# Kernel tuning notes

Hardware: AMD Instinct MI355X
Metric: run time of the kernel (lower is better)

The kernel has to match this reference:

```python
import jax, jax.numpy as jnp
import numpy as np

POOL_RATIOS = [0.5, 0.5, 0.5]
N_NODES = 100000
N_EDGES = 3200000
D = 1443  # hard-coded feature dim in the module


def setup_inputs() -> dict:
    key = jax.random.key(0)
    ks = jax.random.split(key, 6)
    x = jax.random.normal(ks[0], (N_NODES, D), dtype=jnp.float32)
    edge_index = jax.random.randint(ks[1], (2, N_EDGES), 0, N_NODES, dtype=jnp.int64)
    edge_attr = jax.random.uniform(ks[2], (N_EDGES,), dtype=jnp.float32)
    w1 = jax.random.normal(ks[3], (D,), dtype=jnp.float32)
    w2 = jax.random.normal(ks[4], (D,), dtype=jnp.float32)
    w3 = jax.random.normal(ks[5], (D,), dtype=jnp.float32)
    return {"x": x, "edge_index": edge_index, "edge_attr": edge_attr,
            "w1": w1, "w2": w2, "w3": w3}


def _topk_pool(x, w, ratio, n):
    # PyG TopKPooling (single graph, batch = zeros):
    #   score = tanh((x @ attn) / ||attn||); perm = top-k(score, ceil(ratio*N));
    #   x_out = x[perm] * score[perm][:, None]
    s = jnp.tanh((x @ w) / jnp.linalg.norm(w))  # [n]
    k = int(np.ceil(ratio * n))                 # static per layer
    top_s, perm = jax.lax.top_k(s, k)
    return x[perm] * top_s[:, None], k


def reference(x, edge_index, edge_attr, w1, w2, w3):
    # edge_index / edge_attr never influence pooled output (edge filtering is
    # dead code w.r.t. data.x in the original module); scores depend only on x.
    n = x.shape[0]
    for w, r in zip((w1, w2, w3), POOL_RATIOS):
        x, n = _topk_pool(x, w, r, n)
    # global_mean_pool with batch == zeros -> single-graph mean, shape [1, D]
    return jnp.mean(x, axis=0, keepdims=True)
```

## Files before the change

kernel.cpp:

```cpp
#include <hip/hip_runtime.h>
#include <math.h>

#define D_FEAT 1443
#define N0     100000
#define K1SEL  50000
#define K2SEL  25000
#define K3SEL  12500
#define NB     65536
#define EQCAP  4096


__device__ __forceinline__ unsigned fkey(float f) {
    unsigned u = __float_as_uint(f);
    return (u & 0x80000000u) ? ~u : (u | 0x80000000u);
}

__global__ __launch_bounds__(256) void init_kernel(
    const float* __restrict__ w1, const float* __restrict__ w2,
    const float* __restrict__ w3,
    unsigned* __restrict__ hist1, unsigned* __restrict__ hist2,
    int* __restrict__ st, float* __restrict__ out, int outN)
{
    int gid = blockIdx.x * 256 + threadIdx.x;
    int gsz = gridDim.x * 256;
    for (int i = gid; i < NB; i += gsz) { hist1[i] = 0u; hist2[i] = 0u; }
    for (int i = gid; i < outN; i += gsz) out[i] = 0.0f;
    if (blockIdx.x == 0) {
        __shared__ double red[4];
        const float* ws_[3] = { w1, w2, w3 };
        for (int r = 0; r < 3; r++) {
            double nl = 0.0;
            for (int j = threadIdx.x; j < D_FEAT; j += 256) {
                double wv = (double)ws_[r][j]; nl += wv * wv;
            }
            for (int off = 32; off > 0; off >>= 1) nl += __shfl_down(nl, off);
            if ((threadIdx.x & 63) == 0) red[threadIdx.x >> 6] = nl;
            __syncthreads();
            if (threadIdx.x == 0)
                ((float*)st)[8 + r] = (float)(1.0 / sqrt(red[0] + red[1] + red[2] + red[3]));
            __syncthreads();
        }
        if (threadIdx.x < 8) st[threadIdx.x] = 0;
    }
}

__global__ __launch_bounds__(256) void dots_kernel(
    const float* __restrict__ x,
    const float* __restrict__ w1, const float* __restrict__ w2,
    const float* __restrict__ w3,
    float* __restrict__ d2, float* __restrict__ d3,
    unsigned* __restrict__ keys, float* __restrict__ sv,
    unsigned* __restrict__ hist1, const int* __restrict__ st)
{
    int wave = threadIdx.x >> 6, lane = threadIdx.x & 63;
    int row = blockIdx.x * 4 + wave;
    if (row >= N0) return;
    const float* xr = x + (long)row * D_FEAT;
    double a1 = 0.0, a2 = 0.0, a3 = 0.0;
    for (int j = lane; j < D_FEAT; j += 64) {
        double xv = (double)xr[j];
        a1 += xv * (double)w1[j];
        a2 += xv * (double)w2[j];
        a3 += xv * (double)w3[j];
    }
    for (int off = 32; off > 0; off >>= 1) {
        a1 += __shfl_down(a1, off);
        a2 += __shfl_down(a2, off);
        a3 += __shfl_down(a3, off);
    }
    if (lane == 0) {
        d2[row] = (float)a2;
        d3[row] = (float)a3;
        float invN = ((const float*)st)[8];
        float s = tanhf((float)a1 * invN);
        sv[row] = s;
        unsigned key = fkey(s);
        keys[row] = key;
        atomicAdd(&hist1[key >> 16], 1u);
    }
}

__global__ __launch_bounds__(256) void score_kernel(
    const float* __restrict__ dvec, const int* __restrict__ idxIn,
    const float* __restrict__ cumIn, int n, int wIdx,
    unsigned* __restrict__ keys, float* __restrict__ sv,
    unsigned* __restrict__ hist1, const int* __restrict__ st)
{
    int gid = blockIdx.x * 256 + threadIdx.x;
    if (gid >= n) return;
    float invN = ((const float*)st)[8 + wIdx];
    int row = idxIn[gid];
    float c = cumIn[gid];
    float s = tanhf(c * dvec[row] * invN);
    sv[gid] = s;
    unsigned key = fkey(s);
    keys[gid] = key;
    atomicAdd(&hist1[key >> 16], 1u);
}

__global__ __launch_bounds__(256) void hist2_kernel(
    const unsigned* __restrict__ keys, int n,
    unsigned* __restrict__ hist2, const int* __restrict__ st)
{
    int gid = blockIdx.x * 256 + threadIdx.x;
    if (gid >= n) return;
    unsigned p1 = (unsigned)st[0];
    unsigned k = keys[gid];
    if ((k >> 16) == p1) atomicAdd(&hist2[k & 0xFFFFu], 1u);
}

__global__ __launch_bounds__(1024) void pick_kernel(
    const unsigned* __restrict__ hist, int* __restrict__ st, int level, int k0)
{
    __shared__ unsigned csuf[1024];
    int tid = threadIdx.x;
    unsigned kRem = (level == 1) ? (unsigned)k0 : (unsigned)st[2];
    int base = tid * 64;
    unsigned s = 0;
    for (int b = 0; b < 64; b++) s += hist[base + b];
    csuf[tid] = s;
    __syncthreads();
    for (int off = 1; off < 1024; off <<= 1) {
        unsigned v = csuf[tid] + ((tid + off < 1024) ? csuf[tid + off] : 0u);
        __syncthreads();
        csuf[tid] = v;
        __syncthreads();
    }
    unsigned suf = csuf[tid];
    unsigned sufNext = (tid < 1023) ? csuf[tid + 1] : 0u;
    if (suf >= kRem && sufNext < kRem) {
        unsigned acc = sufNext, hsel = 0; int sel = base;
        for (int b = base + 63; b >= base; b--) {
            unsigned h = hist[b];
            acc += h;
            if (acc >= kRem) { sel = b; hsel = h; break; }
        }
        unsigned needNext = kRem - (acc - hsel);
        if (level == 1) {
            st[0] = sel;
            st[2] = (int)needNext;
        } else {
            st[1] = (int)(((unsigned)st[0] << 16) | (unsigned)sel);
            st[2] = (int)needNext;
            st[3] = (int)hsel;
            st[4] = 0;
            st[5] = 0;
        }
    }
}

__global__ __launch_bounds__(256) void compact_kernel(
    const unsigned* __restrict__ keys, const float* __restrict__ sv,
    const int* __restrict__ idxIn, const float* __restrict__ cumIn,
    int n, int* __restrict__ idxOut, float* __restrict__ cumOut,
    int* __restrict__ st,
    unsigned* __restrict__ hist1, unsigned* __restrict__ hist2, int doZero)
{
    int gid = blockIdx.x * 256 + threadIdx.x;
    int gsz = gridDim.x * 256;
    if (doZero) {
        for (int i = gid; i < NB; i += gsz) { hist1[i] = 0u; hist2[i] = 0u; }
    }
    if (gid >= n) return;
    unsigned thr = (unsigned)st[1];
    unsigned key = keys[gid];
    if (key > thr) {
        int pos = atomicAdd(&st[5], 1);
        idxOut[pos] = idxIn ? idxIn[gid] : gid;
        cumOut[pos] = (idxIn ? cumIn[gid] : 1.0f) * sv[gid];
    } else if (key == thr) {
        int e = atomicAdd(&st[4], 1);
        if (e < EQCAP) st[16 + e] = gid;
    }
}

__global__ __launch_bounds__(256) void tie_kernel(
    const float* __restrict__ sv, const int* __restrict__ idxIn,
    const float* __restrict__ cumIn, int k,
    int* __restrict__ idxOut, float* __restrict__ cumOut, int* __restrict__ st)
{
    int cnt = st[4]; if (cnt > EQCAP) cnt = EQCAP;
    int need = st[2];
    int base = k - need;
    for (int e = threadIdx.x; e < cnt; e += 256) {
        int pos = st[16 + e];
        int rank = 0;
        for (int e2 = 0; e2 < cnt; e2++) rank += (st[16 + e2] < pos) ? 1 : 0;
        if (rank < need) {
            idxOut[base + rank] = idxIn ? idxIn[pos] : pos;
            cumOut[base + rank] = (idxIn ? cumIn[pos] : 1.0f) * sv[pos];
        }
    }
}

#define WS_ROWS 64
__global__ __launch_bounds__(256) void wsum_kernel(
    const float* __restrict__ x, const int* __restrict__ idx3,
    const float* __restrict__ cum3, float* __restrict__ out)
{
    int col = blockIdx.x * 256 + threadIdx.x;
    int r0 = blockIdx.y * WS_ROWS;
    int r1 = r0 + WS_ROWS; if (r1 > K3SEL) r1 = K3SEL;
    float acc = 0.0f;
    for (int r = r0; r < r1; r++) {
        int row = idx3[r];
        float wgt = cum3[r];
        if (col < D_FEAT) acc += wgt * x[(long)row * D_FEAT + col];
    }
    if (col < D_FEAT) atomicAdd(&out[col], acc * (1.0f / (float)K3SEL));
}

extern "C" void kernel_launch(void* const* d_in, const int* in_sizes, int n_in,
                              void* d_out, int out_size, void* d_ws, size_t ws_size,
                              hipStream_t stream) {
    const float* x  = (const float*)d_in[0];
    const float* w1 = (const float*)d_in[3];
    const float* w2 = (const float*)d_in[4];
    const float* w3 = (const float*)d_in[5];
    float* out = (float*)d_out;

    float* ws = (float*)d_ws;
    float*    d2    = ws;
    float*    d3    = ws + 100000;
    unsigned* keys  = (unsigned*)(ws + 200000);
    float*    sv    = ws + 300000;
    int*      idx1  = (int*)(ws + 400000);
    float*    cum1  = ws + 450000;
    int*      idx2  = (int*)(ws + 500000);
    float*    cum2  = ws + 525000;
    int*      idx3  = (int*)(ws + 550000);
    float*    cum3  = ws + 562500;
    unsigned* hist1 = (unsigned*)(ws + 575000);
    unsigned* hist2 = (unsigned*)(ws + 575000 + NB);
    int*      st    = (int*)(ws + 575000 + 2 * NB);

    init_kernel<<<dim3(256), dim3(256), 0, stream>>>(w1, w2, w3, hist1, hist2, st, out, out_size);

    dots_kernel<<<dim3(N0 / 4), dim3(256), 0, stream>>>(x, w1, w2, w3, d2, d3,
                                                        keys, sv, hist1, st);

    pick_kernel<<<1, 1024, 0, stream>>>(hist1, st, 1, K1SEL);
    hist2_kernel<<<dim3((N0 + 255) / 256), dim3(256), 0, stream>>>(keys, N0, hist2, st);
    pick_kernel<<<1, 1024, 0, stream>>>(hist2, st, 2, 0);
    compact_kernel<<<dim3((N0 + 255) / 256), dim3(256), 0, stream>>>(
        keys, sv, nullptr, nullptr, N0, idx1, cum1, st, hist1, hist2, 1);
    tie_kernel<<<1, 256, 0, stream>>>(sv, nullptr, nullptr, K1SEL, idx1, cum1, st);

    score_kernel<<<dim3((K1SEL + 255) / 256), dim3(256), 0, stream>>>(
        d2, idx1, cum1, K1SEL, 1, keys, sv, hist1, st);
    pick_kernel<<<1, 1024, 0, stream>>>(hist1, st, 1, K2SEL);
    hist2_kernel<<<dim3((K1SEL + 255) / 256), dim3(256), 0, stream>>>(keys, K1SEL, hist2, st);
    pick_kernel<<<1, 1024, 0, stream>>>(hist2, st, 2, 0);
    compact_kernel<<<dim3((K1SEL + 255) / 256), dim3(256), 0, stream>>>(
        keys, sv, idx1, cum1, K1SEL, idx2, cum2, st, hist1, hist2, 1);
    tie_kernel<<<1, 256, 0, stream>>>(sv, idx1, cum1, K2SEL, idx2, cum2, st);

    score_kernel<<<dim3((K2SEL + 255) / 256), dim3(256), 0, stream>>>(
        d3, idx2, cum2, K2SEL, 2, keys, sv, hist1, st);
    pick_kernel<<<1, 1024, 0, stream>>>(hist1, st, 1, K3SEL);
    hist2_kernel<<<dim3((K2SEL + 255) / 256), dim3(256), 0, stream>>>(keys, K2SEL, hist2, st);
    pick_kernel<<<1, 1024, 0, stream>>>(hist2, st, 2, 0);
    compact_kernel<<<dim3((K2SEL + 255) / 256), dim3(256), 0, stream>>>(
        keys, sv, idx2, cum2, K2SEL, idx3, cum3, st, hist1, hist2, 0);
    tie_kernel<<<1, 256, 0, stream>>>(sv, idx2, cum2, K3SEL, idx3, cum3, st);

    wsum_kernel<<<dim3((D_FEAT + 255) / 256, (K3SEL + WS_ROWS - 1) / WS_ROWS),
                  dim3(256), 0, stream>>>(x, idx3, cum3, out);
}
```

Measured before the change: 1.015 ms.

## Fuse radix top-k threshold search into one block and fold scoring into compaction

Replaces the two-level 16-bit histogram select (hist2 + two pick kernels per layer) with a single-block three-pass 11/11/10-bit radix select that builds the later histograms in shared memory. Next-layer scoring and its first histogram are folded into the compact and tie kernels, writing to separate key/score buffers. This removes the separate score kernel, the large 64K histograms and their zeroing, and several launches per layer. The cost is that one 1024-thread block must scan all keys twice per layer, which serialises work on a single CU.

```diff
diff --git a/kernel.cpp b/kernel.cpp
--- a/kernel.cpp
+++ b/kernel.cpp
@@ -6,7 +6,7 @@
 #define K1SEL  50000
 #define K2SEL  25000
 #define K3SEL  12500
-#define NB     65536
+#define NB1    2048
 #define EQCAP  4096
 
 
@@ -18,12 +18,12 @@
 __global__ __launch_bounds__(256) void init_kernel(
     const float* __restrict__ w1, const float* __restrict__ w2,
     const float* __restrict__ w3,
-    unsigned* __restrict__ hist1, unsigned* __restrict__ hist2,
-    int* __restrict__ st, float* __restrict__ out, int outN)
+    unsigned* __restrict__ hist1, int* __restrict__ st,
+    float* __restrict__ out, int outN)
 {
     int gid = blockIdx.x * 256 + threadIdx.x;
     int gsz = gridDim.x * 256;
-    for (int i = gid; i < NB; i += gsz) { hist1[i] = 0u; hist2[i] = 0u; }
+    for (int i = gid; i < NB1; i += gsz) hist1[i] = 0u;
     for (int i = gid; i < outN; i += gsz) out[i] = 0.0f;
     if (blockIdx.x == 0) {
         __shared__ double red[4];
@@ -76,98 +76,104 @@
         sv[row] = s;
         unsigned key = fkey(s);
         keys[row] = key;
-        atomicAdd(&hist1[key >> 16], 1u);
-    }
-}
-
-__global__ __launch_bounds__(256) void score_kernel(
-    const float* __restrict__ dvec, const int* __restrict__ idxIn,
-    const float* __restrict__ cumIn, int n, int wIdx,
-    unsigned* __restrict__ keys, float* __restrict__ sv,
-    unsigned* __restrict__ hist1, const int* __restrict__ st)
+        atomicAdd(&hist1[key >> 21], 1u);
+    }
+}
+
+__device__ __forceinline__ void pick2048(
+    unsigned* h, unsigned* scan, unsigned kRem,
+    unsigned* selS, unsigned* needS, unsigned* hselS)
+{
+    int tid = threadIdx.x;
+    unsigned h0 = h[2 * tid], h1 = h[2 * tid + 1];
+    scan[tid] = h0 + h1;
+    __syncthreads();
+    for (int off = 1; off < 1024; off <<= 1) {
+        unsigned v = scan[tid] + ((tid + off < 1024) ? scan[tid + off] : 0u);
+        __syncthreads();
+        scan[tid] = v;
+        __syncthreads();
+    }
+    unsigned S  = scan[tid];
+    unsigned Sn = (tid < 1023) ? scan[tid + 1] : 0u;
+    unsigned sufB = S - h0;
+    if (S >= kRem && sufB < kRem)  { *selS = 2u * tid;     *needS = kRem - sufB; *hselS = h0; }
+    if (sufB >= kRem && Sn < kRem) { *selS = 2u * tid + 1; *needS = kRem - Sn;   *hselS = h1; }
+    __syncthreads();
+}
+
+__global__ __launch_bounds__(1024) void fpick_kernel(
+    const unsigned* __restrict__ keys, int n,
+    unsigned* __restrict__ hist1, int* __restrict__ st, int k0)
+{
+    __shared__ unsigned h[NB1];
+    __shared__ unsigned scan[1024];
+    __shared__ unsigned selS, needS, hselS;
+    int tid = threadIdx.x;
+
+    h[2 * tid]     = hist1[2 * tid];
+    h[2 * tid + 1] = hist1[2 * tid + 1];
+    hist1[2 * tid] = 0u; hist1[2 * tid + 1] = 0u;
+    __syncthreads();
+    pick2048(h, scan, (unsigned)k0, &selS, &needS, &hselS);
+    unsigned s1 = selS, kRem2 = needS;
+    __syncthreads();
+
+    h[2 * tid] = 0u; h[2 * tid + 1] = 0u;
+    __syncthreads();
+    for (int i = tid; i < n; i += 1024) {
+        unsigned k = keys[i];
+        if ((k >> 21) == s1) atomicAdd(&h[(k >> 10) & 0x7FFu], 1u);
+    }
+    __syncthreads();
+    pick2048(h, scan, kRem2, &selS, &needS, &hselS);
+    unsigned s2 = selS, kRem3 = needS;
+    unsigned pref = (s1 << 11) | s2;
+    __syncthreads();
+
+    h[2 * tid] = 0u; h[2 * tid + 1] = 0u;
+    __syncthreads();
+    for (int i = tid; i < n; i += 1024) {
+        unsigned k = keys[i];
+        if ((k >> 10) == pref) atomicAdd(&h[k & 0x3FFu], 1u);
+    }
+    __syncthreads();
+    pick2048(h, scan, kRem3, &selS, &needS, &hselS);
+    if (tid == 0) {
+        st[1] = (int)((s1 << 21) | (s2 << 10) | selS);
+        st[2] = (int)needS;
+        st[3] = (int)hselS;
+        st[4] = 0;
+        st[5] = 0;
+    }
+}
+
+__global__ __launch_bounds__(256) void compact_kernel(
+    const unsigned* __restrict__ keysIn, const float* __restrict__ svIn,
+    const int* __restrict__ idxIn, const float* __restrict__ cumIn, int n,
+    int* __restrict__ idxOut, float* __restrict__ cumOut,
+    int* __restrict__ st,
+    const float* __restrict__ dNext, unsigned* __restrict__ keysOut,
+    float* __restrict__ svOut, unsigned* __restrict__ hist1, int wIdx)
 {
     int gid = blockIdx.x * 256 + threadIdx.x;
     if (gid >= n) return;
-    float invN = ((const float*)st)[8 + wIdx];
-    int row = idxIn[gid];
-    float c = cumIn[gid];
-    float s = tanhf(c * dvec[row] * invN);
-    sv[gid] = s;
-    unsigned key = fkey(s);
-    keys[gid] = key;
-    atomicAdd(&hist1[key >> 16], 1u);
-}
-
-__global__ __launch_bounds__(256) void hist2_kernel(
-    const unsigned* __restrict__ keys, int n,
-    unsigned* __restrict__ hist2, const int* __restrict__ st)
-{
-    int gid = blockIdx.x * 256 + threadIdx.x;
-    if (gid >= n) return;
-    unsigned p1 = (unsigned)st[0];
-    unsigned k = keys[gid];
-    if ((k >> 16) == p1) atomicAdd(&hist2[k & 0xFFFFu], 1u);
-}
-
-__global__ __launch_bounds__(1024) void pick_kernel(
-    const unsigned* __restrict__ hist, int* __restrict__ st, int level, int k0)
-{
-    __shared__ unsigned csuf[1024];
-    int tid = threadIdx.x;
-    unsigned kRem = (level == 1) ? (unsigned)k0 : (unsigned)st[2];
-    int base = tid * 64;
-    unsigned s = 0;
-    for (int b = 0; b < 64; b++) s += hist[base + b];
-    csuf[tid] = s;
-    __syncthreads();
-    for (int off = 1; off < 1024; off <<= 1) {
-        unsigned v = csuf[tid] + ((tid + off < 1024) ? csuf[tid + off] : 0u);
-        __syncthreads();
-        csuf[tid] = v;
-        __syncthreads();
-    }
-    unsigned suf = csuf[tid];
-    unsigned sufNext = (tid < 1023) ? csuf[tid + 1] : 0u;
-    if (suf >= kRem && sufNext < kRem) {
-        unsigned acc = sufNext, hsel = 0; int sel = base;
-        for (int b = base + 63; b >= base; b--) {
-            unsigned h = hist[b];
-            acc += h;
-            if (acc >= kRem) { sel = b; hsel = h; break; }
-        }
-        unsigned needNext = kRem - (acc - hsel);
-        if (level == 1) {
-            st[0] = sel;
-            st[2] = (int)needNext;
-        } else {
-            st[1] = (int)(((unsigned)st[0] << 16) | (unsigned)sel);
-            st[2] = (int)needNext;
-            st[3] = (int)hsel;
-            st[4] = 0;
-            st[5] = 0;
-        }
-    }
-}
-
-__global__ __launch_bounds__(256) void compact_kernel(
-    const unsigned* __restrict__ keys, const float* __restrict__ sv,
-    const int* __restrict__ idxIn, const float* __restrict__ cumIn,
-    int n, int* __restrict__ idxOut, float* __restrict__ cumOut,
-    int* __restrict__ st,
-    unsigned* __restrict__ hist1, unsigned* __restrict__ hist2, int doZero)
-{
-    int gid = blockIdx.x * 256 + threadIdx.x;
-    int gsz = gridDim.x * 256;
-    if (doZero) {
-        for (int i = gid; i < NB; i += gsz) { hist1[i] = 0u; hist2[i] = 0u; }
-    }
-    if (gid >= n) return;
     unsigned thr = (unsigned)st[1];
-    unsigned key = keys[gid];
+    unsigned key = keysIn[gid];
     if (key > thr) {
         int pos = atomicAdd(&st[5], 1);
-        idxOut[pos] = idxIn ? idxIn[gid] : gid;
-        cumOut[pos] = (idxIn ? cumIn[gid] : 1.0f) * sv[gid];
+        int row = idxIn ? idxIn[gid] : gid;
+        float c = (idxIn ? cumIn[gid] : 1.0f) * svIn[gid];
+        idxOut[pos] = row;
+        cumOut[pos] = c;
+        if (dNext) {
+            float invN = ((const float*)st)[8 + wIdx];
+            float s = tanhf(c * dNext[row] * invN);
+            svOut[pos] = s;
+            unsigned k2 = fkey(s);
+            keysOut[pos] = k2;
+            atomicAdd(&hist1[k2 >> 21], 1u);
+        }
     } else if (key == thr) {
         int e = atomicAdd(&st[4], 1);
         if (e < EQCAP) st[16 + e] = gid;
@@ -175,9 +181,11 @@
 }
 
 __global__ __launch_bounds__(256) void tie_kernel(
-    const float* __restrict__ sv, const int* __restrict__ idxIn,
+    const float* __restrict__ svIn, const int* __restrict__ idxIn,
     const float* __restrict__ cumIn, int k,
-    int* __restrict__ idxOut, float* __restrict__ cumOut, int* __restrict__ st)
+    int* __restrict__ idxOut, float* __restrict__ cumOut, int* __restrict__ st,
+    const float* __restrict__ dNext, unsigned* __restrict__ keysOut,
+    float* __restrict__ svOut, unsigned* __restrict__ hist1, int wIdx)
 {
     int cnt = st[4]; if (cnt > EQCAP) cnt = EQCAP;
     int need = st[2];
@@ -187,8 +195,18 @@
         int rank = 0;
         for (int e2 = 0; e2 < cnt; e2++) rank += (st[16 + e2] < pos) ? 1 : 0;
         if (rank < need) {
-            idxOut[base + rank] = idxIn ? idxIn[pos] : pos;
-            cumOut[base + rank] = (idxIn ? cumIn[pos] : 1.0f) * sv[pos];
+            int row = idxIn ? idxIn[pos] : pos;
+            float c = (idxIn ? cumIn[pos] : 1.0f) * svIn[pos];
+            idxOut[base + rank] = row;
+            cumOut[base + rank] = c;
+            if (dNext) {
+                float invN = ((const float*)st)[8 + wIdx];
+                float s = tanhf(c * dNext[row] * invN);
+                svOut[base + rank] = s;
+                unsigned k2 = fkey(s);
+                keysOut[base + rank] = k2;
+                atomicAdd(&hist1[k2 >> 21], 1u);
+            }
         }
     }
 }
@@ -222,47 +240,46 @@
     float* ws = (float*)d_ws;
     float*    d2    = ws;
     float*    d3    = ws + 100000;
-    unsigned* keys  = (unsigned*)(ws + 200000);
-    float*    sv    = ws + 300000;
+    unsigned* keysA = (unsigned*)(ws + 200000);
+    float*    svA   = ws + 300000;
     int*      idx1  = (int*)(ws + 400000);
     float*    cum1  = ws + 450000;
-    int*      idx2  = (int*)(ws + 500000);
-    float*    cum2  = ws + 525000;
-    int*      idx3  = (int*)(ws + 550000);
-    float*    cum3  = ws + 562500;
-    unsigned* hist1 = (unsigned*)(ws + 575000);
-    unsigned* hist2 = (unsigned*)(ws + 575000 + NB);
-    int*      st    = (int*)(ws + 575000 + 2 * NB);
-
-    init_kernel<<<dim3(256), dim3(256), 0, stream>>>(w1, w2, w3, hist1, hist2, st, out, out_size);
+    unsigned* keysB = (unsigned*)(ws + 500000);
+    float*    svB   = ws + 550000;
+    int*      idx2  = (int*)(ws + 600000);
+    float*    cum2  = ws + 625000;
+    unsigned* keysC = (unsigned*)(ws + 650000);
+    float*    svC   = ws + 675000;
+    int*      idx3  = (int*)(ws + 700000);
+    float*    cum3  = ws + 712500;
+    unsigned* hist1 = (unsigned*)(ws + 725000);
+    int*      st    = (int*)(ws + 725000 + NB1);
+
+    init_kernel<<<dim3(16), dim3(256), 0, stream>>>(w1, w2, w3, hist1, st, out, out_size);
 
     dots_kernel<<<dim3(N0 / 4), dim3(256), 0, stream>>>(x, w1, w2, w3, d2, d3,
-                                                        keys, sv, hist1, st);
-
-    pick_kernel<<<1, 1024, 0, stream>>>(hist1, st, 1, K1SEL);
-    hist2_kernel<<<dim3((N0 + 255) / 256), dim3(256), 0, stream>>>(keys, N0, hist2, st);
-    pick_kernel<<<1, 1024, 0, stream>>>(hist2, st, 2, 0);
+                                                        keysA, svA, hist1, st);
+
+    fpick_kernel<<<1, 1024, 0, stream>>>(keysA, N0, hist1, st, K1SEL);
     compact_kernel<<<dim3((N0 + 255) / 256), dim3(256), 0, stream>>>(
-        keys, sv, nullptr, nullptr, N0, idx1, cum1, st, hist1, hist2, 1);
-    tie_kernel<<<1, 256, 0, stream>>>(sv, nullptr, nullptr, K1SEL, idx1, cum1, st);
-
-    score_kernel<<<dim3((K1SEL + 255) / 256), dim3(256), 0, stream>>>(
-        d2, idx1, cum1, K1SEL, 1, keys, sv, hist1, st);
-    pick_kernel<<<1, 1024, 0, stream>>>(hist1, st, 1, K2SEL);
-    hist2_kernel<<<dim3((K1SEL + 255) / 256), dim3(256), 0, stream>>>(keys, K1SEL, hist2, st);
-    pick_kernel<<<1, 1024, 0, stream>>>(hist2, st, 2, 0);
+        keysA, svA, nullptr, nullptr, N0, idx1, cum1, st,
+        d2, keysB, svB, hist1, 1);
+    tie_kernel<<<1, 256, 0, stream>>>(svA, nullptr, nullptr, K1SEL, idx1, cum1, st,
+                                      d2, keysB, svB, hist1, 1);
+
+    fpick_kernel<<<1, 1024, 0, stream>>>(keysB, K1SEL, hist1, st, K2SEL);
     compact_kernel<<<dim3((K1SEL + 255) / 256), dim3(256), 0, stream>>>(
-        keys, sv, idx1, cum1, K1SEL, idx2, cum2, st, hist1, hist2, 1);
-    tie_kernel<<<1, 256, 0, stream>>>(sv, idx1, cum1, K2SEL, idx2, cum2, st);
-
-    score_kernel<<<dim3((K2SEL + 255) / 256), dim3(256), 0, stream>>>(
-        d3, idx2, cum2, K2SEL, 2, keys, sv, hist1, st);
-    pick_kernel<<<1, 1024, 0, stream>>>(hist1, st, 1, K3SEL);
-    hist2_kernel<<<dim3((K2SEL + 255) / 256), dim3(256), 0, stream>>>(keys, K2SEL, hist2, st);
-    pick_kernel<<<1, 1024, 0, stream>>>(hist2, st, 2, 0);
+        keysB, svB, idx1, cum1, K1SEL, idx2, cum2, st,
+        d3, keysC, svC, hist1, 2);
+    tie_kernel<<<1, 256, 0, stream>>>(svB, idx1, cum1, K2SEL, idx2, cum2, st,
+                                      d3, keysC, svC, hist1, 2);
+
+    fpick_kernel<<<1, 1024, 0, stream>>>(keysC, K2SEL, hist1, st, K3SEL);
     compact_kernel<<<dim3((K2SEL + 255) / 256), dim3(256), 0, stream>>>(
-        keys, sv, idx2, cum2, K2SEL, idx3, cum3, st, hist1, hist2, 0);
-    tie_kernel<<<1, 256, 0, stream>>>(sv, idx2, cum2, K3SEL, idx3, cum3, st);
+        keysC, svC, idx2, cum2, K2SEL, idx3, cum3, st,
+        nullptr, nullptr, nullptr, nullptr, 0);
+    tie_kernel<<<1, 256, 0, stream>>>(svC, idx2, cum2, K3SEL, idx3, cum3, st,
+                                      nullptr, nullptr, nullptr, nullptr, 0);
 
     wsum_kernel<<<dim3((D_FEAT + 255) / 256, (K3SEL + WS_ROWS - 1) / WS_ROWS),
                   dim3(256), 0, stream>>>(x, idx3, cum3, out);
```

Measured after the change: 1.264 ms. 24.5% more time.
